# Kernel tuning notes

Measured on AMD Instinct MI355X. Metric: run time of the kernel, lower is better.

## Reference

```python
import jax, jax.numpy as jnp
import numpy as np

B, N, F_IN, DEG = 8, 4096, 8, 8
E = B * N * DEG
MAX_RADIUS, NUM_BASIS, HIDDEN = 3.0, 10, 64
MUL0, MUL1 = 32, 16  # irreps_potential = '32x0e + 16x1o'
W_NUMEL = F_IN * (MUL0 + MUL1)  # 384


def setup_inputs() -> dict:
    key = jax.random.key(0)
    k1, k2, k3, k4, k5, k6 = jax.random.split(key, 6)
    node_features = jax.random.normal(k1, (B, N, F_IN), jnp.float32)
    pos = 4.0 * jax.random.uniform(k2, (B, N, 3), dtype=jnp.float32)  # box so many pairs fall inside max_radius
    # static-shape stand-in for radius_graph: DEG random neighbors per node, within each graph, no self loops
    src = jax.random.randint(k3, (B, N * DEG), 0, N)
    off = jax.random.randint(k4, (B, N * DEG), 1, N)
    dst = (src + off) % N
    boff = (jnp.arange(B) * N)[:, None]
    edge_src = (src + boff).reshape(-1).astype(jnp.int32)
    edge_dst = (dst + boff).reshape(-1).astype(jnp.int32)
    W1 = jax.random.normal(k5, (NUM_BASIS, HIDDEN), jnp.float32)
    W2 = jax.random.normal(k6, (HIDDEN, W_NUMEL), jnp.float32)
    return {"node_features": node_features, "pos": pos, "edge_src": edge_src,
            "edge_dst": edge_dst, "W1": W1, "W2": W2}


def _forward(node_features, pos, edge_src, edge_dst, W1, W2):
    pos_flat = pos.reshape(-1, 3)            # [B*N, 3]
    x_flat = node_features.reshape(-1, F_IN)  # [B*N, F_IN]
    edge_vec = pos_flat[edge_src] - pos_flat[edge_dst]  # [E,3]
    r = jnp.sqrt(jnp.sum(edge_vec * edge_vec, axis=1) + 1e-18)  # [E]

    # soft_one_hot_linspace(r, 0, R, num_basis, basis='smooth_finite', cutoff=True) * sqrt(num_basis)
    values = jnp.linspace(0.0, MAX_RADIUS, NUM_BASIS + 2)[1:-1]
    step = values[1] - values[0]
    d = (r[:, None] - values[None, :]) / step
    inside = jnp.abs(d) < 1.0
    y = jnp.where(inside, jnp.maximum(1.0 - d * d, 1e-7), 1.0)
    emb = jnp.where(inside, 1.14136 * jnp.exp(2.0) * jnp.exp(-1.0 / y), 0.0)
    emb = emb * (NUM_BASIS ** 0.5)           # [E, num_basis]

    # soft_unit_step(10 * (1 - r/R))
    t = 10.0 * (1.0 - r / MAX_RADIUS)
    w_cut = jnp.where(t > 0.0, jnp.exp(-1.0 / jnp.where(t > 0.0, t, 1.0)), 0.0)

    # spherical harmonics lmax=2, normalize=True, 'component' normalization
    u = edge_vec / r[:, None]
    ux, uy, uz = u[:, 0], u[:, 1], u[:, 2]
    sh1 = jnp.sqrt(3.0) * u                  # l=1 (component norm); sh0 == 1
    c15 = np.sqrt(15.0)
    sh2 = jnp.stack([c15 * ux * uy, c15 * uy * uz, 0.5 * np.sqrt(5.0) * (3 * uz * uz - 1.0),
                     c15 * ux * uz, 0.5 * c15 * (ux * ux - uy * uy)], axis=1)
    del sh2  # 2e couples 0e input only to 2e, which is absent from '32x0e+16x1o' -> no path

    # FullyConnectedNet([num_basis, hidden, weight_numel], silu) -> per-edge TP weights
    h = jax.nn.silu(emb @ (W1 / np.sqrt(NUM_BASIS)))
    w = h @ (W2 / np.sqrt(HIDDEN))           # [E, 384]
    wA = w[:, : F_IN * MUL0].reshape(-1, F_IN, MUL0)
    wB = w[:, F_IN * MUL0:].reshape(-1, F_IN, MUL1)

    # FullyConnectedTensorProduct (uvw), shared_weights=False, path norm 1/sqrt(fan_in)
    x_src = x_flat[edge_src]                 # gather [E, F_IN]
    inv = 1.0 / np.sqrt(F_IN)
    out0 = jnp.einsum('eu,euw->ew', x_src, wA) * inv            # 0e x 0e -> 32x0e
    out1 = jnp.einsum('eu,ei,euw->ewi', x_src, sh1, wB) * inv   # 0e x 1o -> 16x1o
    potential = jnp.concatenate([out0, out1.reshape(-1, 3 * MUL1)], axis=1)  # [E, 80]

    # scatter-add to destination nodes
    nodes = jax.ops.segment_sum(w_cut[:, None] * potential, edge_dst, num_segments=B * N)
    psi = nodes[:, :3].reshape(B, N, 3)
    curl = jnp.stack([psi[..., 2] - psi[..., 1],
                      psi[..., 0] - psi[..., 2],
                      psi[..., 1] - psi[..., 0]], axis=-1)       # [B, N, 3]
    return curl


def reference(node_features, pos, edge_src, edge_dst, W1, W2):
    return _forward(node_features, pos, edge_src, edge_dst, W1, W2)
```

## Files before the change

kernel.cpp:

```cpp
#include <hip/hip_runtime.h>
#include <hip/hip_fp16.h>


#define THREADS 256
#define RTAB 2048
#define ROWH 64

__global__ __launch_bounds__(THREADS) void se3_build_table(
    const float* __restrict__ W1,
    const float* __restrict__ W2,
    __half* __restrict__ T)
{
    __shared__ float sW1[10 * 65];
    for (int t = threadIdx.x; t < 640; t += THREADS) {
        int j = t >> 6, k = t & 63;
        sW1[j * 65 + k] = W1[t];
    }
    __syncthreads();

    int g = blockIdx.x * THREADS + threadIdx.x;
    if (g >= RTAB * 24) return;
    int i = g / 24;
    int j = g - i * 24;
    int u = j / 3, c = j - u * 3;

    float r = 3.0f * (float)i / (float)(RTAB - 1);

    float psi = 0.0f;
    float t10 = 10.0f - (10.0f / 3.0f) * r;
    if (t10 > 0.0f) {
        const float C0 = 8.43357306907549f;
        float q  = r * (11.0f / 3.0f);
        int   jf = (int)q;
        float da = q - (float)jf;
        float db = da - 1.0f;
        float ya = fmaxf(1.0f - da * da, 1e-7f);
        float yb = fmaxf(1.0f - db * db, 1e-7f);
        int ja = jf - 1, jb = jf;
        float ea = (ja >= 0) ? C0 * __expf(-1.0f / ya) : 0.0f;
        float eb = (jb <= 9) ? C0 * __expf(-1.0f / yb) : 0.0f;
        int jac = ja < 0 ? 0 : ja;
        int jbc = jb > 9 ? 9 : jb;
        const float* w1a = sW1 + jac * 65;
        const float* w1b = sW1 + jbc * 65;
        const float* w2  = W2 + u * 32 + c;

        float acc = 0.0f;
#pragma unroll 8
        for (int k = 0; k < 64; ++k) {
            float pre = ea * w1a[k] + eb * w1b[k];
            float h   = pre * __builtin_amdgcn_rcpf(1.0f + __expf(-pre));
            acc += h * w2[k * 384];
        }
        psi = acc * __expf(-1.0f / t10) * 0.04419417382415922f;
    }

    __half hv = __float2half(psi);
    T[(size_t)i * ROWH + 2 * j] = hv;
    if (i > 0) T[(size_t)(i - 1) * ROWH + 2 * j + 1] = hv;
}

__global__ __launch_bounds__(THREADS) void se3_edge_kernel(
    const float* __restrict__ x,
    const float* __restrict__ pos,
    const int*   __restrict__ esrc,
    const int*   __restrict__ edst,
    const __half* __restrict__ T,
    float*       __restrict__ outbuf,
    int E, int ncopies, int outN)
{
    int e = blockIdx.x * THREADS + threadIdx.x;
    if (e >= E) return;

    int s = esrc[e];
    int d = edst[e];

    float ex = pos[3 * s + 0] - pos[3 * d + 0];
    float ey = pos[3 * s + 1] - pos[3 * d + 1];
    float ez = pos[3 * s + 2] - pos[3 * d + 2];
    float r  = sqrtf(ex * ex + ey * ey + ez * ez + 1e-18f);

    if (r >= 3.0f) return;

    float tq = r * ((float)(RTAB - 1) / 3.0f);
    int   i  = (int)tq;
    if (i > RTAB - 2) i = RTAB - 2;
    float f  = tq - (float)i;

    const float4* rowp = reinterpret_cast<const float4*>(T + (size_t)i * ROWH);
    const float4* xf   = reinterpret_cast<const float4*>(x + 8 * (size_t)s);
    float4 xA = xf[0];
    float4 xB = xf[1];
    float xs[8] = {xA.x, xA.y, xA.z, xA.w, xB.x, xB.y, xB.z, xB.w};

    float p[3] = {0.0f, 0.0f, 0.0f};
#pragma unroll
    for (int qi = 0; qi < 6; ++qi) {
        float4 v = rowp[qi];
        const __half2* h2 = reinterpret_cast<const __half2*>(&v);
#pragma unroll
        for (int m = 0; m < 4; ++m) {
            int j = 4 * qi + m;
            int u = j / 3, c = j - 3 * u;
            float2 ab = __half22float2(h2[m]);
            float val = fmaf(f, ab.y - ab.x, ab.x);
            p[c] = fmaf(xs[u], val, p[c]);
        }
    }

    float* ob = outbuf + (size_t)(blockIdx.x % ncopies) * outN + 3 * d;
    atomicAdd(ob + 0, p[2] - p[1]);
    atomicAdd(ob + 1, p[0] - p[2]);
    atomicAdd(ob + 2, p[1] - p[0]);
}

__global__ __launch_bounds__(THREADS) void se3_reduce_kernel(
    const float* __restrict__ ws, float* __restrict__ out,
    int outN4, int ncopies)
{
    int idx = blockIdx.x * THREADS + threadIdx.x;
    if (idx >= outN4) return;
    const float4* w = reinterpret_cast<const float4*>(ws);
    float4 acc = w[idx];
    for (int c = 1; c < ncopies; ++c) {
        float4 v = w[(size_t)c * outN4 + idx];
        acc.x += v.x; acc.y += v.y; acc.z += v.z; acc.w += v.w;
    }
    reinterpret_cast<float4*>(out)[idx] = acc;
}

extern "C" void kernel_launch(void* const* d_in, const int* in_sizes, int n_in,
                              void* d_out, int out_size, void* d_ws, size_t ws_size,
                              hipStream_t stream) {
    const float* x    = (const float*)d_in[0];
    const float* pos  = (const float*)d_in[1];
    const int*   esrc = (const int*)d_in[2];
    const int*   edst = (const int*)d_in[3];
    const float* W1   = (const float*)d_in[4];
    const float* W2   = (const float*)d_in[5];
    float* out = (float*)d_out;

    int E    = in_sizes[2];
    int outN = out_size;

    size_t tableBytes = (size_t)RTAB * ROWH * sizeof(__half);
    __half* T = (__half*)d_ws;

    int ncopies = 1;
    if (ws_size > tableBytes) {
        size_t rem = ws_size - tableBytes;
        int nc = (int)(rem / ((size_t)outN * sizeof(float)));
        if (nc > 8) nc = 8;
        if (nc < 1) nc = 1;
        ncopies = nc;
    }

    int buildBlocks = (RTAB * 24 + THREADS - 1) / THREADS;
    se3_build_table<<<buildBlocks, THREADS, 0, stream>>>(W1, W2, T);

    int edgeBlocks = (E + THREADS - 1) / THREADS;
    if (ncopies >= 2) {
        float* copies = (float*)((char*)d_ws + tableBytes);
        hipMemsetAsync(copies, 0, (size_t)ncopies * outN * sizeof(float), stream);
        se3_edge_kernel<<<edgeBlocks, THREADS, 0, stream>>>(
            x, pos, esrc, edst, T, copies, E, ncopies, outN);
        int outN4 = outN / 4;
        se3_reduce_kernel<<<(outN4 + THREADS - 1) / THREADS, THREADS, 0, stream>>>(
            copies, out, outN4, ncopies);
    } else {
        hipMemsetAsync(out, 0, (size_t)outN * sizeof(float), stream);
        se3_edge_kernel<<<edgeBlocks, THREADS, 0, stream>>>(
            x, pos, esrc, edst, T, out, E, 1, outN);
    }
}
```

Measured before the change: 105.6 us.

## Stage radial table in LDS, pack node records, fuse memset into build kernel

New measurement: 105.9 us. About the same (+0.3%).

```diff
diff --git a/kernel.cpp b/kernel.cpp
--- a/kernel.cpp
+++ b/kernel.cpp
@@ -3,83 +3,118 @@
 
 
 #define THREADS 256
-#define RTAB 2048
-#define ROWH 64
-
-__global__ __launch_bounds__(THREADS) void se3_build_table(
+#define RTAB 1024
+#define NCOPIES 8
+
+#define TAB_OFF   0u
+#define TAB_BYTES (RTAB * 24 * 2u)
+#define NODE_OFF  65536u
+#define NODE_BYTES(nNodes) ((unsigned)(nNodes) * 64u)
+
+__global__ __launch_bounds__(THREADS) void se3_build(
     const float* __restrict__ W1,
     const float* __restrict__ W2,
-    __half* __restrict__ T)
+    const float* __restrict__ pos,
+    const float* __restrict__ x,
+    __half*  __restrict__ T,
+    float4*  __restrict__ nodes,
+    float4*  __restrict__ copies,
+    int nNodes, int copies4)
 {
     __shared__ float sW1[10 * 65];
+    __shared__ float sW2[64 * 24];
+
     for (int t = threadIdx.x; t < 640; t += THREADS) {
         int j = t >> 6, k = t & 63;
         sW1[j * 65 + k] = W1[t];
     }
+    for (int t = threadIdx.x; t < 64 * 24; t += THREADS) {
+        int k = t / 24, j = t - 24 * k;
+        int u = j / 3, c = j - 3 * u;
+        sW2[t] = W2[k * 384 + u * 32 + c];
+    }
     __syncthreads();
 
     int g = blockIdx.x * THREADS + threadIdx.x;
-    if (g >= RTAB * 24) return;
-    int i = g / 24;
-    int j = g - i * 24;
-    int u = j / 3, c = j - u * 3;
-
-    float r = 3.0f * (float)i / (float)(RTAB - 1);
-
-    float psi = 0.0f;
-    float t10 = 10.0f - (10.0f / 3.0f) * r;
-    if (t10 > 0.0f) {
-        const float C0 = 8.43357306907549f;
-        float q  = r * (11.0f / 3.0f);
-        int   jf = (int)q;
-        float da = q - (float)jf;
-        float db = da - 1.0f;
-        float ya = fmaxf(1.0f - da * da, 1e-7f);
-        float yb = fmaxf(1.0f - db * db, 1e-7f);
-        int ja = jf - 1, jb = jf;
-        float ea = (ja >= 0) ? C0 * __expf(-1.0f / ya) : 0.0f;
-        float eb = (jb <= 9) ? C0 * __expf(-1.0f / yb) : 0.0f;
-        int jac = ja < 0 ? 0 : ja;
-        int jbc = jb > 9 ? 9 : jb;
-        const float* w1a = sW1 + jac * 65;
-        const float* w1b = sW1 + jbc * 65;
-        const float* w2  = W2 + u * 32 + c;
-
-        float acc = 0.0f;
+    int nthreads = gridDim.x * THREADS;
+
+    if (g < RTAB * 24) {
+        int i = g / 24;
+        int j = g - i * 24;
+        float r = 3.0f * (float)i / (float)(RTAB - 1);
+
+        float psi = 0.0f;
+        float t10 = 10.0f - (10.0f / 3.0f) * r;
+        if (t10 > 0.0f) {
+            const float C0 = 8.43357306907549f;
+            float q  = r * (11.0f / 3.0f);
+            int   jf = (int)q;
+            float da = q - (float)jf;
+            float db = da - 1.0f;
+            float ya = fmaxf(1.0f - da * da, 1e-7f);
+            float yb = fmaxf(1.0f - db * db, 1e-7f);
+            int ja = jf - 1, jb = jf;
+            float ea = (ja >= 0) ? C0 * __expf(-1.0f / ya) : 0.0f;
+            float eb = (jb <= 9) ? C0 * __expf(-1.0f / yb) : 0.0f;
+            int jac = ja < 0 ? 0 : ja;
+            int jbc = jb > 9 ? 9 : jb;
+            const float* w1a = sW1 + jac * 65;
+            const float* w1b = sW1 + jbc * 65;
+
+            float acc = 0.0f;
 #pragma unroll 8
-        for (int k = 0; k < 64; ++k) {
-            float pre = ea * w1a[k] + eb * w1b[k];
-            float h   = pre * __builtin_amdgcn_rcpf(1.0f + __expf(-pre));
-            acc += h * w2[k * 384];
-        }
-        psi = acc * __expf(-1.0f / t10) * 0.04419417382415922f;
-    }
-
-    __half hv = __float2half(psi);
-    T[(size_t)i * ROWH + 2 * j] = hv;
-    if (i > 0) T[(size_t)(i - 1) * ROWH + 2 * j + 1] = hv;
-}
-
-__global__ __launch_bounds__(THREADS) void se3_edge_kernel(
-    const float* __restrict__ x,
-    const float* __restrict__ pos,
-    const int*   __restrict__ esrc,
-    const int*   __restrict__ edst,
-    const __half* __restrict__ T,
-    float*       __restrict__ outbuf,
+            for (int k = 0; k < 64; ++k) {
+                float pre = ea * w1a[k] + eb * w1b[k];
+                float h   = pre * __builtin_amdgcn_rcpf(1.0f + __expf(-pre));
+                acc = fmaf(h, sW2[k * 24 + j], acc);
+            }
+            psi = acc * __expf(-1.0f / t10) * 0.04419417382415922f;
+        }
+        T[i * 24 + j] = __float2half(psi);
+    }
+
+    for (int n = g; n < nNodes; n += nthreads) {
+        const float* p = pos + 3 * (size_t)n;
+        const float4* xf = reinterpret_cast<const float4*>(x + 8 * (size_t)n);
+        float4 rec0 = make_float4(p[0], p[1], p[2], 0.0f);
+        nodes[n * 4 + 0] = rec0;
+        nodes[n * 4 + 1] = xf[0];
+        nodes[n * 4 + 2] = xf[1];
+    }
+
+    float4 z = make_float4(0.f, 0.f, 0.f, 0.f);
+    for (int i = g; i < copies4; i += nthreads) copies[i] = z;
+}
+
+__global__ __launch_bounds__(THREADS) void se3_edge(
+    const float4* __restrict__ nodes,
+    const int*    __restrict__ esrc,
+    const int*    __restrict__ edst,
+    const float4* __restrict__ Tg,
+    float*        __restrict__ outbuf,
     int E, int ncopies, int outN)
 {
+    __shared__ __align__(16) __half sT[RTAB * 24];
+
+    float4* sT4 = reinterpret_cast<float4*>(sT);
+#pragma unroll
+    for (int q = 0; q < (RTAB * 24 * 2 / 16) / THREADS; ++q)
+        sT4[threadIdx.x + q * THREADS] = Tg[threadIdx.x + q * THREADS];
+    __syncthreads();
+
     int e = blockIdx.x * THREADS + threadIdx.x;
     if (e >= E) return;
 
     int s = esrc[e];
     int d = edst[e];
 
-    float ex = pos[3 * s + 0] - pos[3 * d + 0];
-    float ey = pos[3 * s + 1] - pos[3 * d + 1];
-    float ez = pos[3 * s + 2] - pos[3 * d + 2];
+    float4 ps = nodes[s * 4 + 0];
+    float4 xA = nodes[s * 4 + 1];
+    float4 xB = nodes[s * 4 + 2];
+    float4 pd = nodes[d * 4 + 0];
+
+    float ex = ps.x - pd.x, ey = ps.y - pd.y, ez = ps.z - pd.z;
     float r  = sqrtf(ex * ex + ey * ey + ez * ez + 1e-18f);
-
     if (r >= 3.0f) return;
 
     float tq = r * ((float)(RTAB - 1) / 3.0f);
@@ -87,46 +122,66 @@
     if (i > RTAB - 2) i = RTAB - 2;
     float f  = tq - (float)i;
 
-    const float4* rowp = reinterpret_cast<const float4*>(T + (size_t)i * ROWH);
-    const float4* xf   = reinterpret_cast<const float4*>(x + 8 * (size_t)s);
-    float4 xA = xf[0];
-    float4 xB = xf[1];
     float xs[8] = {xA.x, xA.y, xA.z, xA.w, xB.x, xB.y, xB.z, xB.w};
-
-    float p[3] = {0.0f, 0.0f, 0.0f};
+    float p0 = 0.f, p1 = 0.f, p2 = 0.f;
+
+    const uint2* row_a = reinterpret_cast<const uint2*>(sT + i * 24);
+    const uint2* row_b = reinterpret_cast<const uint2*>(sT + (i + 1) * 24);
 #pragma unroll
-    for (int qi = 0; qi < 6; ++qi) {
-        float4 v = rowp[qi];
-        const __half2* h2 = reinterpret_cast<const __half2*>(&v);
-#pragma unroll
-        for (int m = 0; m < 4; ++m) {
-            int j = 4 * qi + m;
-            int u = j / 3, c = j - 3 * u;
-            float2 ab = __half22float2(h2[m]);
-            float val = fmaf(f, ab.y - ab.x, ab.x);
-            p[c] = fmaf(xs[u], val, p[c]);
+    for (int m = 0; m < 6; ++m) {
+        union { uint2 u; __half2 h[2]; } A, B;
+        A.u = row_a[m];
+        B.u = row_b[m];
+        float2 a0 = __half22float2(A.h[0]), a1 = __half22float2(A.h[1]);
+        float2 b0 = __half22float2(B.h[0]), b1 = __half22float2(B.h[1]);
+        {
+            const int j = 4 * m + 0, u = j / 3, c = j - 3 * u;
+            float v = fmaf(f, b0.x - a0.x, a0.x);
+            if (c == 0) p0 = fmaf(xs[u], v, p0);
+            else if (c == 1) p1 = fmaf(xs[u], v, p1);
+            else p2 = fmaf(xs[u], v, p2);
+        }
+        {
+            const int j = 4 * m + 1, u = j / 3, c = j - 3 * u;
+            float v = fmaf(f, b0.y - a0.y, a0.y);
+            if (c == 0) p0 = fmaf(xs[u], v, p0);
+            else if (c == 1) p1 = fmaf(xs[u], v, p1);
+            else p2 = fmaf(xs[u], v, p2);
+        }
+        {
+            const int j = 4 * m + 2, u = j / 3, c = j - 3 * u;
+            float v = fmaf(f, b1.x - a1.x, a1.x);
+            if (c == 0) p0 = fmaf(xs[u], v, p0);
+            else if (c == 1) p1 = fmaf(xs[u], v, p1);
+            else p2 = fmaf(xs[u], v, p2);
+        }
+        {
+            const int j = 4 * m + 3, u = j / 3, c = j - 3 * u;
+            float v = fmaf(f, b1.y - a1.y, a1.y);
+            if (c == 0) p0 = fmaf(xs[u], v, p0);
+            else if (c == 1) p1 = fmaf(xs[u], v, p1);
+            else p2 = fmaf(xs[u], v, p2);
         }
     }
 
     float* ob = outbuf + (size_t)(blockIdx.x % ncopies) * outN + 3 * d;
-    atomicAdd(ob + 0, p[2] - p[1]);
-    atomicAdd(ob + 1, p[0] - p[2]);
-    atomicAdd(ob + 2, p[1] - p[0]);
-}
-
-__global__ __launch_bounds__(THREADS) void se3_reduce_kernel(
-    const float* __restrict__ ws, float* __restrict__ out,
+    atomicAdd(ob + 0, p2 - p1);
+    atomicAdd(ob + 1, p0 - p2);
+    atomicAdd(ob + 2, p1 - p0);
+}
+
+__global__ __launch_bounds__(THREADS) void se3_reduce(
+    const float4* __restrict__ ws, float4* __restrict__ out,
     int outN4, int ncopies)
 {
     int idx = blockIdx.x * THREADS + threadIdx.x;
     if (idx >= outN4) return;
-    const float4* w = reinterpret_cast<const float4*>(ws);
-    float4 acc = w[idx];
+    float4 acc = ws[idx];
     for (int c = 1; c < ncopies; ++c) {
-        float4 v = w[(size_t)c * outN4 + idx];
+        float4 v = ws[(size_t)c * outN4 + idx];
         acc.x += v.x; acc.y += v.y; acc.z += v.z; acc.w += v.w;
     }
-    reinterpret_cast<float4*>(out)[idx] = acc;
+    out[idx] = acc;
 }
 
 extern "C" void kernel_launch(void* const* d_in, const int* in_sizes, int n_in,
@@ -138,38 +193,36 @@
     const int*   edst = (const int*)d_in[3];
     const float* W1   = (const float*)d_in[4];
     const float* W2   = (const float*)d_in[5];
-    float* out = (float*)d_out;
-
-    int E    = in_sizes[2];
-    int outN = out_size;
-
-    size_t tableBytes = (size_t)RTAB * ROWH * sizeof(__half);
-    __half* T = (__half*)d_ws;
-
-    int ncopies = 1;
-    if (ws_size > tableBytes) {
-        size_t rem = ws_size - tableBytes;
-        int nc = (int)(rem / ((size_t)outN * sizeof(float)));
-        if (nc > 8) nc = 8;
-        if (nc < 1) nc = 1;
-        ncopies = nc;
-    }
-
-    int buildBlocks = (RTAB * 24 + THREADS - 1) / THREADS;
-    se3_build_table<<<buildBlocks, THREADS, 0, stream>>>(W1, W2, T);
+
+    int E      = in_sizes[2];
+    int outN   = out_size;
+    int nNodes = in_sizes[1] / 3;
+
+    char* ws = (char*)d_ws;
+    __half* T      = (__half*)(ws + TAB_OFF);
+    float4* nodes  = (float4*)(ws + NODE_OFF);
+    size_t  copOff = (size_t)NODE_OFF + NODE_BYTES(nNodes);
+    float*  copies = (float*)(ws + copOff);
+
+    size_t need = copOff + (size_t)NCOPIES * outN * sizeof(float);
+    int ncopies = (ws_size >= need) ? NCOPIES : 1;
+    if (ncopies == 1) {
+        copies = (float*)d_out;
+        hipMemsetAsync(d_out, 0, (size_t)outN * sizeof(float), stream);
+    }
+
+    int copies4 = (ncopies == 1) ? 0 : (ncopies * outN) / 4;
+    int buildBlocks = (nNodes + THREADS - 1) / THREADS;
+    se3_build<<<buildBlocks, THREADS, 0, stream>>>(
+        W1, W2, pos, x, T, nodes, (float4*)copies, nNodes, copies4);
 
     int edgeBlocks = (E + THREADS - 1) / THREADS;
-    if (ncopies >= 2) {
-        float* copies = (float*)((char*)d_ws + tableBytes);
-        hipMemsetAsync(copies, 0, (size_t)ncopies * outN * sizeof(float), stream);
-        se3_edge_kernel<<<edgeBlocks, THREADS, 0, stream>>>(
-            x, pos, esrc, edst, T, copies, E, ncopies, outN);
+    se3_edge<<<edgeBlocks, THREADS, 0, stream>>>(
+        nodes, esrc, edst, (const float4*)T, copies, E, ncopies, outN);
+
+    if (ncopies > 1) {
         int outN4 = outN / 4;
-        se3_reduce_kernel<<<(outN4 + THREADS - 1) / THREADS, THREADS, 0, stream>>>(
-            copies, out, outN4, ncopies);
-    } else {
-        hipMemsetAsync(out, 0, (size_t)outN * sizeof(float), stream);
-        se3_edge_kernel<<<edgeBlocks, THREADS, 0, stream>>>(
-            x, pos, esrc, edst, T, out, E, 1, outN);
-    }
-}
+        se3_reduce<<<(outN4 + THREADS - 1) / THREADS, THREADS, 0, stream>>>(
+            (const float4*)copies, (float4*)d_out, outN4, ncopies);
+    }
+}
```
